# Performance work log

Hardware: AMD Instinct MI355X
Metric: run time of the kernel (lower is better)

Reference implementation:

```python
import jax, jax.numpy as jnp
import numpy as np

H = 16          # num attention heads (== num kv heads here)
D = 128         # head_dim
HID = 2048      # hidden_size = H * D
THETA = 10000.0
SCALE = 1.0 / (D ** 0.5)
EPS = 1e-8


def rotate_half(x):
    x1, x2 = x[..., : D // 2], x[..., D // 2 :]
    return jnp.concatenate((-x2, x1), axis=-1)


def rope_tables(seq_len):
    inv_freq = 1.0 / (THETA ** (jnp.arange(0, D, 2, dtype=jnp.float32) / D))
    freqs = jnp.outer(jnp.arange(seq_len, dtype=jnp.float32), inv_freq)  # [S, D/2]
    emb = jnp.concatenate((freqs, freqs), axis=-1)                        # [S, D]
    return jnp.cos(emb), jnp.sin(emb)


def setup_inputs() -> dict:
    key = jax.random.key(0)
    ks = jax.random.split(key, 10)
    B, S = 1, 2048
    hidden_states = jax.random.normal(ks[0], (B, S, HID), jnp.float32) * 0.02
    position_ids = jnp.tile(jnp.arange(S, dtype=jnp.int32)[None, :], (B, 1))
    # additive causal mask, shape (B, 1, S, S) as asserted in the torch forward
    causal = jnp.tril(jnp.ones((S, S), dtype=bool))
    attention_mask = jnp.where(causal, 0.0, -1e9).astype(jnp.float32)[None, None]
    attention_mask = jnp.tile(attention_mask, (B, 1, 1, 1))
    Wq = jax.random.normal(ks[1], (HID, HID), jnp.float32) * 0.02
    bq = jax.random.normal(ks[2], (HID,), jnp.float32) * 0.02
    Wk = jax.random.normal(ks[3], (HID, HID), jnp.float32) * 0.02
    bk = jax.random.normal(ks[4], (HID,), jnp.float32) * 0.02
    Wo = jax.random.normal(ks[5], (HID, HID), jnp.float32) * 0.02
    beta = jax.random.normal(ks[6], (1,), jnp.float32)
    M = jax.random.normal(ks[7], (H, D, D), jnp.float32) * 0.02
    z = jax.random.uniform(ks[8], (H, D), jnp.float32) * 100.0 + 1.0  # positive accumulator
    return {
        "hidden_states": hidden_states,
        "attention_mask": attention_mask,
        "position_ids": position_ids,
        "Wq": Wq, "bq": bq, "Wk": Wk, "bk": bk, "Wo": Wo,
        "beta": beta, "M": M, "z": z,
    }


def reference(hidden_states, attention_mask, position_ids, Wq, bq, Wk, bk, Wo, beta, M, z):
    B, S, _ = hidden_states.shape
    # projections (NOTE: source uses q_proj for value_states too -- reproduced faithfully)
    q = (hidden_states @ Wq + bq).reshape(B, S, H, D).transpose(0, 2, 1, 3)  # [B,H,S,D]
    k = (hidden_states @ Wk + bk).reshape(B, S, H, D).transpose(0, 2, 1, 3)
    v = q  # value_states = q_proj(hidden_states), no RoPE applied to values

    cos, sin = rope_tables(S)
    cos = cos[position_ids][:, None]  # [B,1,S,D]
    sin = sin[position_ids][:, None]
    qr = q * cos + rotate_half(q) * sin
    kr = k * cos + rotate_half(k) * sin

    # --- compressive memory retrieval (with pre-update M, z) ---
    sq = jax.nn.elu(qr) + 1.0                                  # [B,H,S,D]
    mem_num = jnp.einsum('bhsd,hde->bhse', sq, M)              # [B,H,S,D]
    mem_den = jnp.einsum('bhsd,hd->bhs', sq, z)[..., None] + EPS
    memory_output = mem_num / mem_den

    # --- memory update: outer-product accumulation ---
    sk = jax.nn.elu(kr) + 1.0
    M_new = M + jnp.einsum('bhsd,bhse->hde', sk, v)
    z_new = z + sk.sum(axis=(0, 2))

    # --- local attention (SDPA with additive mask, dropout 0) ---
    scores = jnp.einsum('bhsd,bhtd->bhst', qr, kr) * SCALE + attention_mask
    probs = jax.nn.softmax(scores, axis=-1)
    attn_output = jnp.einsum('bhst,bhtd->bhsd', probs, v)

    # --- long-term memory injection: sigmoid-gated blend ---
    g = jax.nn.sigmoid(beta)[0]
    combined = g * memory_output + (1.0 - g) * attn_output     # [B,H,S,D]
    combined = combined.transpose(0, 2, 1, 3).reshape(B, S, HID)
    final_output = combined @ Wo
    return (final_output, M_new, z_new)
```

## Files before the change

### kernel.cpp

```cpp
#include <hip/hip_runtime.h>
#include <hip/hip_bf16.h>


#define S_LEN 2048
#define HID 2048
#define NH 16
#define HD 128
#define SCALE_QK 0.088388347648318447f

typedef __attribute__((ext_vector_type(8))) short bf16x8;
typedef __attribute__((ext_vector_type(4))) float f32x4;

__device__ __forceinline__ short f2bf(float f) {
  __hip_bfloat16 h = __float2bfloat16(f);
  return __builtin_bit_cast(short, h);
}
__device__ __forceinline__ float bf2f(short s) {
  unsigned int u = ((unsigned int)(unsigned short)s) << 16;
  return __builtin_bit_cast(float, u);
}
__device__ __forceinline__ void gload16(const void* g, void* l) {
  __builtin_amdgcn_global_load_lds(
      (const __attribute__((address_space(1))) void*)g,
      (__attribute__((address_space(3))) void*)l, 16, 0, 0);
}

__global__ __launch_bounds__(256) void f32_to_bf16_kernel(
    const float* __restrict__ in, short* __restrict__ out) {
  size_t i = (size_t)(blockIdx.x * 256 + threadIdx.x) * 8;
  float4 a = *reinterpret_cast<const float4*>(in + i);
  float4 b = *reinterpret_cast<const float4*>(in + i + 4);
  alignas(16) short t[8] = {f2bf(a.x), f2bf(a.y), f2bf(a.z), f2bf(a.w),
                            f2bf(b.x), f2bf(b.y), f2bf(b.z), f2bf(b.w)};
  *reinterpret_cast<int4*>(out + i) = *reinterpret_cast<int4*>(t);
}

__global__ __launch_bounds__(256) void transpose_f2b_kernel(
    const float* __restrict__ in, short* __restrict__ out, int R, int C) {
  __shared__ float t[32][33];
  size_t bo = (size_t)blockIdx.z * R * C;
  int r0 = blockIdx.y * 32, c0 = blockIdx.x * 32;
  int tx = threadIdx.x & 31, ty = threadIdx.x >> 5;
#pragma unroll
  for (int i = 0; i < 4; ++i)
    t[ty + i * 8][tx] = in[bo + (size_t)(r0 + ty + i * 8) * C + c0 + tx];
  __syncthreads();
#pragma unroll
  for (int i = 0; i < 4; ++i)
    out[bo + (size_t)(c0 + ty + i * 8) * R + r0 + tx] = f2bf(t[tx][ty + i * 8]);
}

__global__ __launch_bounds__(256) void transpose_b2b_kernel(
    const short* __restrict__ in, short* __restrict__ out, int R, int C) {
  __shared__ short t[32][33];
  int r0 = blockIdx.y * 32, c0 = blockIdx.x * 32;
  int tx = threadIdx.x & 31, ty = threadIdx.x >> 5;
#pragma unroll
  for (int i = 0; i < 4; ++i)
    t[ty + i * 8][tx] = in[(size_t)(r0 + ty + i * 8) * C + c0 + tx];
  __syncthreads();
#pragma unroll
  for (int i = 0; i < 4; ++i)
    out[(size_t)(c0 + ty + i * 8) * R + r0 + tx] = t[tx][ty + i * 8];
}

__global__ __launch_bounds__(256) void tables_kernel(
    const int* __restrict__ pos_ids, float* __restrict__ cost,
    float* __restrict__ sint) {
  int idx = blockIdx.x * 256 + threadIdx.x;
  int s = idx >> 6, j = idx & 63;
  float pos = (float)pos_ids[s];
  float inv = powf(10000.0f, -((float)j) / 64.0f);
  float a = pos * inv;
  cost[idx] = cosf(a);
  sint[idx] = sinf(a);
}

__global__ __launch_bounds__(256) void gemm_bt_dual_kernel(
    const short* __restrict__ A, const short* __restrict__ BT,
    const float* __restrict__ bias0, const float* __restrict__ bias1,
    float* __restrict__ C0, float* __restrict__ C1) {
  __shared__ short As[128 * 64];
  __shared__ short Bs[128 * 64];
  const int K = 2048;
  const int tid = threadIdx.x;
  const int wave = tid >> 6, lane = tid & 63;
  const int g = lane >> 4, l15 = lane & 15;
  const int wm = (wave >> 1) * 64, wn = (wave & 1) * 64;
  const int row0 = blockIdx.x * 128;
  const int colg0 = blockIdx.y * 128;

  const int ld_r = wave * 32 + (lane >> 3);
  const int ld_c = (lane & 7) * 8;
  const short* Ag = A + (size_t)(row0 + ld_r) * K + ld_c;
  const short* Bg = BT + (size_t)(colg0 + ld_r) * K + ld_c;
  short* Al = As + wave * 2048;
  short* Bl = Bs + wave * 2048;

  f32x4 acc[4][4] = {};
  for (int kt = 0; kt < K; kt += 64) {
    __syncthreads();
#pragma unroll
    for (int i = 0; i < 4; ++i) {
      gload16(Ag + kt + (size_t)i * 8 * K, Al + i * 512);
      gload16(Bg + kt + (size_t)i * 8 * K, Bl + i * 512);
    }
    __syncthreads();
#pragma unroll
    for (int ks = 0; ks < 2; ++ks) {
      bf16x8 a[4], b[4];
#pragma unroll
      for (int m = 0; m < 4; ++m)
        a[m] = *reinterpret_cast<bf16x8*>(
            reinterpret_cast<char*>(As) + (wm + m * 16 + l15) * 128 +
            (ks * 32 + g * 8) * 2);
#pragma unroll
      for (int n = 0; n < 4; ++n)
        b[n] = *reinterpret_cast<bf16x8*>(
            reinterpret_cast<char*>(Bs) + (wn + n * 16 + l15) * 128 +
            (ks * 32 + g * 8) * 2);
#pragma unroll
      for (int m = 0; m < 4; ++m)
#pragma unroll
        for (int n = 0; n < 4; ++n)
          acc[m][n] = __builtin_amdgcn_mfma_f32_16x16x32_bf16(a[m], b[n],
                                                              acc[m][n], 0, 0, 0);
    }
  }

  float* C = (colg0 < 2048) ? C0 : C1;
  const float* bias = (colg0 < 2048) ? bias0 : bias1;
  const int col0 = (colg0 < 2048) ? colg0 : colg0 - 2048;
#pragma unroll
  for (int m = 0; m < 4; ++m)
#pragma unroll
    for (int n = 0; n < 4; ++n) {
      int row = row0 + wm + m * 16 + g * 4;
      int col = col0 + wn + n * 16 + l15;
      float bv = bias ? bias[col] : 0.0f;
#pragma unroll
      for (int r = 0; r < 4; ++r)
        C[(size_t)(row + r) * 2048 + col] = acc[m][n][r] + bv;
    }
}

__global__ __launch_bounds__(256) void rope_kernel(
    const float* __restrict__ qf, const float* __restrict__ kf,
    const float* __restrict__ cost, const float* __restrict__ sint,
    short* __restrict__ qr, short* __restrict__ kr, short* __restrict__ sq,
    short* __restrict__ sk, short* __restrict__ v) {
  int s = blockIdx.x;
  int hd = threadIdx.x * 8;
  int d = hd & 127;
  bool lo = d < 64;
  size_t base = (size_t)s * HID + hd;
  size_t pb = lo ? base + 64 : base - 64;
  int tb = s * 64 + (hd & 63);
  alignas(16) short oqr[8], okr[8], osq[8], osk[8], ov[8];
#pragma unroll
  for (int j = 0; j < 8; ++j) {
    float c = cost[tb + j], sn = sint[tb + j];
    float q = qf[base + j], qp = qf[pb + j];
    float k = kf[base + j], kp = kf[pb + j];
    float rq = lo ? -qp : qp;
    float rk = lo ? -kp : kp;
    float qrv = q * c + rq * sn;
    float krv = k * c + rk * sn;
    oqr[j] = f2bf(qrv);
    okr[j] = f2bf(krv);
    osq[j] = f2bf(qrv > 0.0f ? qrv + 1.0f : __expf(qrv));
    osk[j] = f2bf(krv > 0.0f ? krv + 1.0f : __expf(krv));
    ov[j] = f2bf(q);
  }
  *reinterpret_cast<int4*>(qr + base) = *reinterpret_cast<int4*>(oqr);
  *reinterpret_cast<int4*>(kr + base) = *reinterpret_cast<int4*>(okr);
  *reinterpret_cast<int4*>(sq + base) = *reinterpret_cast<int4*>(osq);
  *reinterpret_cast<int4*>(sk + base) = *reinterpret_cast<int4*>(osk);
  *reinterpret_cast<int4*>(v + base) = *reinterpret_cast<int4*>(ov);
}

__global__ __launch_bounds__(256) void attn_kernel(
    const short* __restrict__ qr, const short* __restrict__ kr,
    const short* __restrict__ vT, const short* __restrict__ sq,
    const short* __restrict__ MT, const float* __restrict__ z,
    const float* __restrict__ beta, short* __restrict__ comb) {
  __shared__ short k_s[2][64 * 128];
  __shared__ short v_s[2][128 * 64];
  __shared__ short p_s[4][16 * 64];
  const int tid = threadIdx.x;
  const int wave = tid >> 6, lane = tid & 63;
  const int g = lane >> 4, l15 = lane & 15;
  const int bid = blockIdx.x;
  const int h = bid & 15;
  const int u = bid >> 4;
  const int qt = (u < 16) ? (2 * u) : (31 - 2 * (u - 16));
  const int q0 = qt * 64;
  const int ntiles = qt + 1;

  const int krow_b = wave * 16 + (lane >> 4);
  const int vrow_b = wave * 32 + (lane >> 3);
#define STAGE_TILE(B, T0)                                                     \
  {                                                                           \
    _Pragma("unroll") for (int i = 0; i < 4; ++i) {                           \
      int rk = krow_b + i * 4;                                                \
      int ck = (lane & 15) ^ (rk & 7);                                        \
      gload16(kr + (size_t)((T0) + rk) * HID + h * HD + ck * 8,               \
              &k_s[B][0] + wave * 2048 + i * 512);                            \
      int rv = vrow_b + i * 8;                                                \
      int cv = (lane & 7) ^ (rv & 7);                                         \
      gload16(vT + (size_t)(h * HD + rv) * S_LEN + (T0) + cv * 8,             \
              &v_s[B][0] + wave * 2048 + i * 512);                            \
    }                                                                         \
  }

  bf16x8 qf[4];
#pragma unroll
  for (int ks = 0; ks < 4; ++ks) {
    int row = q0 + wave * 16 + l15;
    qf[ks] = *reinterpret_cast<const bf16x8*>(qr + (size_t)row * HID + h * HD +
                                              ks * 32 + g * 8);
  }

  STAGE_TILE(0, 0);
  __syncthreads();

  f32x4 o[8] = {};
  float m_run[4], l_run[4];
#pragma unroll
  for (int r = 0; r < 4; ++r) {
    m_run[r] = -3.0e38f;
    l_run[r] = 0.0f;
  }

  for (int kt = 0; kt < ntiles; ++kt) {
    const int cur = kt & 1;
    if (kt + 1 < ntiles) STAGE_TILE(cur ^ 1, (kt + 1) * 64);

    f32x4 sfr[4] = {};
    __builtin_amdgcn_s_setprio(1);
#pragma unroll
    for (int n = 0; n < 4; ++n) {
#pragma unroll
      for (int ks = 0; ks < 4; ++ks) {
        int rr = n * 16 + l15;
        int off = (rr * 256 + (ks * 32 + g * 8) * 2) ^ ((rr & 7) << 4);
        bf16x8 b =
            *reinterpret_cast<bf16x8*>(reinterpret_cast<char*>(k_s[cur]) + off);
        sfr[n] = __builtin_amdgcn_mfma_f32_16x16x32_bf16(qf[ks], b, sfr[n], 0,
                                                         0, 0);
      }
    }
    __builtin_amdgcn_s_setprio(0);

    const bool diag = (kt == qt);
#pragma unroll
    for (int r = 0; r < 4; ++r) {
      const int srow = q0 + wave * 16 + g * 4 + r;
      float mx = m_run[r];
#pragma unroll
      for (int n = 0; n < 4; ++n) {
        float val = sfr[n][r] * SCALE_QK;
        if (diag) {
          int t = kt * 64 + n * 16 + l15;
          val = (t <= srow) ? val : -3.0e38f;
        }
        sfr[n][r] = val;
        mx = fmaxf(mx, val);
      }
      mx = fmaxf(mx, __shfl_xor(mx, 1));
      mx = fmaxf(mx, __shfl_xor(mx, 2));
      mx = fmaxf(mx, __shfl_xor(mx, 4));
      mx = fmaxf(mx, __shfl_xor(mx, 8));
      float sum = 0.0f;
#pragma unroll
      for (int n = 0; n < 4; ++n) {
        float p = __expf(sfr[n][r] - mx);
        sfr[n][r] = p;
        sum += p;
      }
      sum += __shfl_xor(sum, 1);
      sum += __shfl_xor(sum, 2);
      sum += __shfl_xor(sum, 4);
      sum += __shfl_xor(sum, 8);
      float f = __expf(m_run[r] - mx);
      l_run[r] = l_run[r] * f + sum;
      m_run[r] = mx;
#pragma unroll
      for (int n = 0; n < 8; ++n) o[n][r] *= f;
    }

    char* pw = reinterpret_cast<char*>(p_s[wave]);
#pragma unroll
    for (int n = 0; n < 4; ++n)
#pragma unroll
      for (int r = 0; r < 4; ++r) {
        int rl = g * 4 + r;
        int off = (rl * 128 + (n * 16 + l15) * 2) ^ ((rl & 7) << 4);
        *reinterpret_cast<short*>(pw + off) = f2bf(sfr[n][r]);
      }

    __builtin_amdgcn_s_setprio(1);
#pragma unroll
    for (int ks = 0; ks < 2; ++ks) {
      int offp = (l15 * 128 + (ks * 32 + g * 8) * 2) ^ ((l15 & 7) << 4);
      bf16x8 pa = *reinterpret_cast<bf16x8*>(pw + offp);
#pragma unroll
      for (int n = 0; n < 8; ++n) {
        int rr = n * 16 + l15;
        int off = (rr * 128 + (ks * 32 + g * 8) * 2) ^ ((rr & 7) << 4);
        bf16x8 vb =
            *reinterpret_cast<bf16x8*>(reinterpret_cast<char*>(v_s[cur]) + off);
        o[n] = __builtin_amdgcn_mfma_f32_16x16x32_bf16(pa, vb, o[n], 0, 0, 0);
      }
    }
    __builtin_amdgcn_s_setprio(0);

    __syncthreads();
  }
#undef STAGE_TILE

  short* mt_s = &k_s[0][0];
#pragma unroll
  for (int i = 0; i < 8; ++i) {
    int c = tid + 256 * i;
    int r = c >> 4, kc = c & 15;
    int4 d = *reinterpret_cast<const int4*>(MT + (size_t)h * 16384 + r * 128 +
                                            kc * 8);
    *reinterpret_cast<int4*>(reinterpret_cast<char*>(mt_s) +
                             ((r * 256 + kc * 16) ^ ((r & 7) << 4))) = d;
  }
  __syncthreads();

  bf16x8 af[4];
#pragma unroll
  for (int ks = 0; ks < 4; ++ks) {
    int row = q0 + wave * 16 + l15;
    af[ks] = *reinterpret_cast<const bf16x8*>(sq + (size_t)row * HID + h * HD +
                                              ks * 32 + g * 8);
  }
  f32x4 acc2[8] = {};
#pragma unroll
  for (int ks = 0; ks < 4; ++ks) {
#pragma unroll
    for (int n = 0; n < 8; ++n) {
      int rr = n * 16 + l15;
      int off = (rr * 256 + (ks * 32 + g * 8) * 2) ^ ((rr & 7) << 4);
      bf16x8 b =
          *reinterpret_cast<bf16x8*>(reinterpret_cast<char*>(mt_s) + off);
      acc2[n] = __builtin_amdgcn_mfma_f32_16x16x32_bf16(af[ks], b, acc2[n], 0,
                                                        0, 0);
    }
  }

  float den[4];
#pragma unroll
  for (int r = 0; r < 4; ++r) {
    int row = q0 + wave * 16 + g * 4 + r;
    bf16x8 sv =
        *reinterpret_cast<const bf16x8*>(sq + (size_t)row * HID + h * HD +
                                         l15 * 8);
    float part = 0.0f;
#pragma unroll
    for (int j = 0; j < 8; ++j) part += bf2f(sv[j]) * z[h * HD + l15 * 8 + j];
    part += __shfl_xor(part, 1);
    part += __shfl_xor(part, 2);
    part += __shfl_xor(part, 4);
    part += __shfl_xor(part, 8);
    den[r] = part + 1e-8f;
  }

  float gv = 1.0f / (1.0f + __expf(-beta[0]));
#pragma unroll
  for (int n = 0; n < 8; ++n)
#pragma unroll
    for (int r = 0; r < 4; ++r) {
      int row = q0 + wave * 16 + g * 4 + r;
      int col = n * 16 + l15;
      float mem = acc2[n][r] / den[r];
      float at = o[n][r] / l_run[r];
      comb[(size_t)row * HID + h * HD + col] = f2bf(gv * mem + (1.0f - gv) * at);
    }
}

__global__ __launch_bounds__(256) void mnew_part_kernel(
    const short* __restrict__ skT, const short* __restrict__ vT,
    float* __restrict__ part) {
  const int sp = blockIdx.x;
  const int h = blockIdx.y;
  const int tid = threadIdx.x;
  const int wave = tid >> 6, lane = tid & 63;
  const int g = lane >> 4, l15 = lane & 15;
  f32x4 acc[2][8] = {};
  for (int ks = sp * 8; ks < sp * 8 + 8; ++ks) {
    bf16x8 a[2];
#pragma unroll
    for (int m = 0; m < 2; ++m) {
      int dd = wave * 32 + m * 16 + l15;
      a[m] = *reinterpret_cast<const bf16x8*>(skT + (size_t)(h * HD + dd) * S_LEN +
                                              ks * 32 + g * 8);
    }
#pragma unroll
    for (int n = 0; n < 8; ++n) {
      int e = n * 16 + l15;
      bf16x8 b = *reinterpret_cast<const bf16x8*>(
          vT + (size_t)(h * HD + e) * S_LEN + ks * 32 + g * 8);
#pragma unroll
      for (int m = 0; m < 2; ++m)
        acc[m][n] =
            __builtin_amdgcn_mfma_f32_16x16x32_bf16(a[m], b, acc[m][n], 0, 0, 0);
    }
  }
#pragma unroll
  for (int m = 0; m < 2; ++m)
#pragma unroll
    for (int n = 0; n < 8; ++n)
#pragma unroll
      for (int r = 0; r < 4; ++r) {
        int dd = wave * 32 + m * 16 + g * 4 + r;
        int e = n * 16 + l15;
        part[(size_t)(sp * 16 + h) * 16384 + (size_t)dd * 128 + e] =
            acc[m][n][r];
      }
}

__global__ __launch_bounds__(256) void mnew_reduce_kernel(
    const float* __restrict__ part, const float* __restrict__ Mold,
    float* __restrict__ Mout) {
  int idx = blockIdx.x * 256 + threadIdx.x;
  int j4 = idx * 4;
  int h = j4 >> 14;
  int rem = j4 & 16383;
  float4 a = *reinterpret_cast<const float4*>(Mold + j4);
#pragma unroll
  for (int s = 0; s < 8; ++s) {
    float4 p = *reinterpret_cast<const float4*>(
        part + ((size_t)(s * 16 + h) << 14) + rem);
    a.x += p.x;
    a.y += p.y;
    a.z += p.z;
    a.w += p.w;
  }
  *reinterpret_cast<float4*>(Mout + j4) = a;
}

__global__ __launch_bounds__(256) void znew_kernel(const short* __restrict__ skT,
                                                   const float* __restrict__ z,
                                                   float* __restrict__ out) {
  int row = blockIdx.x;
  int tid = threadIdx.x;
  bf16x8 vv = *reinterpret_cast<const bf16x8*>(skT + (size_t)row * S_LEN + tid * 8);
  float s = 0.0f;
#pragma unroll
  for (int j = 0; j < 8; ++j) s += bf2f(vv[j]);
#pragma unroll
  for (int off = 1; off < 64; off <<= 1) s += __shfl_xor(s, off);
  __shared__ float wsum[4];
  if ((tid & 63) == 0) wsum[tid >> 6] = s;
  __syncthreads();
  if (tid == 0) out[row] = z[row] + wsum[0] + wsum[1] + wsum[2] + wsum[3];
}

extern "C" void kernel_launch(void* const* d_in, const int* in_sizes, int n_in,
                              void* d_out, int out_size, void* d_ws,
                              size_t ws_size, hipStream_t stream) {
  const float* hs = (const float*)d_in[0];
  const int* pos = (const int*)d_in[2];
  const float* Wq = (const float*)d_in[3];
  const float* bq = (const float*)d_in[4];
  const float* Wk = (const float*)d_in[5];
  const float* bk = (const float*)d_in[6];
  const float* Wo = (const float*)d_in[7];
  const float* beta = (const float*)d_in[8];
  const float* Mm = (const float*)d_in[9];
  const float* z = (const float*)d_in[10];
  float* out = (float*)d_out;

  char* ws = (char*)d_ws;
  const size_t MB = 1u << 20;
  float* q_f32 = (float*)(ws + 0);
  float* k_f32 = (float*)(ws + 16 * MB);
  short* hs_b = (short*)(ws + 32 * MB);
  short* WqkT = (short*)(ws + 40 * MB);
  short* WoT = (short*)(ws + 56 * MB);
  short* qr = (short*)(ws + 64 * MB);
  short* kr = (short*)(ws + 72 * MB);
  short* sq = (short*)(ws + 80 * MB);
  short* vT = (short*)(ws + 88 * MB);
  short* MT = (short*)(ws + 96 * MB);
  float* cost = (float*)(ws + 96 * MB + 512 * 1024);
  float* sint = (float*)(ws + 97 * MB);
  short* comb = (short*)k_f32;
  short* sk = hs_b;
  short* v = WqkT;
  short* skT = WqkT + 4 * 1024 * 1024;
  float* mpart = q_f32;

  f32_to_bf16_kernel<<<2048, 256, 0, stream>>>(hs, hs_b);
  transpose_f2b_kernel<<<dim3(64, 64, 1), 256, 0, stream>>>(Wq, WqkT, 2048, 2048);
  transpose_f2b_kernel<<<dim3(64, 64, 1), 256, 0, stream>>>(
      Wk, WqkT + 4 * 1024 * 1024, 2048, 2048);
  transpose_f2b_kernel<<<dim3(64, 64, 1), 256, 0, stream>>>(Wo, WoT, 2048, 2048);
  transpose_f2b_kernel<<<dim3(4, 4, 16), 256, 0, stream>>>(Mm, MT, 128, 128);
  tables_kernel<<<512, 256, 0, stream>>>(pos, cost, sint);

  gemm_bt_dual_kernel<<<dim3(16, 32), 256, 0, stream>>>(hs_b, WqkT, bq, bk,
                                                        q_f32, k_f32);
  rope_kernel<<<2048, 256, 0, stream>>>(q_f32, k_f32, cost, sint, qr, kr, sq, sk,
                                        v);
  transpose_b2b_kernel<<<dim3(64, 64, 1), 256, 0, stream>>>(v, vT, 2048, 2048);
  transpose_b2b_kernel<<<dim3(64, 64, 1), 256, 0, stream>>>(sk, skT, 2048, 2048);

  attn_kernel<<<512, 256, 0, stream>>>(qr, kr, vT, sq, MT, z, beta, comb);
  gemm_bt_dual_kernel<<<dim3(16, 16), 256, 0, stream>>>(comb, WoT, nullptr,
                                                        nullptr, out, out);
  mnew_part_kernel<<<dim3(8, 16), 256, 0, stream>>>(skT, vT, mpart);
  mnew_reduce_kernel<<<256, 256, 0, stream>>>(mpart, Mm, out + 4194304);
  znew_kernel<<<2048, 256, 0, stream>>>(skT, z, out + 4194304 + 16 * 128 * 128);
}
```

Measured before the change: 362.1 us.

## Fuse RoPE epilogue into QK projection GEMM and double-buffer GEMM LDS loads

Folds the bias add, rotary embedding, ELU+1 feature map and bf16 conversion into the epilogue of the Q/K projection GEMM. The tile is staged through shared memory so each thread can reach its rotate-half partner, which removes the fp32 q/k round trip through global memory and one kernel launch. Both GEMMs now double-buffer their LDS tiles, prefetching the next K-slice while the current one feeds the MFMAs. The cost is 64KB+ of LDS per block, which may lower occupancy, plus a reorganised workspace layout.

```diff
diff --git a/kernel.cpp b/kernel.cpp
--- a/kernel.cpp
+++ b/kernel.cpp
@@ -76,12 +76,13 @@
   sint[idx] = sinf(a);
 }
 
-__global__ __launch_bounds__(256) void gemm_bt_dual_kernel(
+__global__ __launch_bounds__(256) void gemm_qk_rope_kernel(
     const short* __restrict__ A, const short* __restrict__ BT,
-    const float* __restrict__ bias0, const float* __restrict__ bias1,
-    float* __restrict__ C0, float* __restrict__ C1) {
-  __shared__ short As[128 * 64];
-  __shared__ short Bs[128 * 64];
+    const float* __restrict__ bq, const float* __restrict__ bk,
+    const float* __restrict__ cost, const float* __restrict__ sint,
+    short* __restrict__ qr, short* __restrict__ kr, short* __restrict__ sq,
+    short* __restrict__ sk, short* __restrict__ v) {
+  __shared__ __align__(16) char smem[67584];
   const int K = 2048;
   const int tid = threadIdx.x;
   const int wave = tid >> 6, lane = tid & 63;
@@ -94,31 +95,36 @@
   const int ld_c = (lane & 7) * 8;
   const short* Ag = A + (size_t)(row0 + ld_r) * K + ld_c;
   const short* Bg = BT + (size_t)(colg0 + ld_r) * K + ld_c;
-  short* Al = As + wave * 2048;
-  short* Bl = Bs + wave * 2048;
+
+#define GSTAGE(BUF, KT)                                                       \
+  {                                                                           \
+    _Pragma("unroll") for (int i = 0; i < 4; ++i) {                           \
+      gload16(Ag + (size_t)(KT) * 64 + (size_t)i * 8 * 2048,                  \
+              smem + (BUF) * 32768 + wave * 4096 + i * 1024);                 \
+      gload16(Bg + (size_t)(KT) * 64 + (size_t)i * 8 * 2048,                  \
+              smem + (BUF) * 32768 + 16384 + wave * 4096 + i * 1024);         \
+    }                                                                         \
+  }
 
   f32x4 acc[4][4] = {};
-  for (int kt = 0; kt < K; kt += 64) {
-    __syncthreads();
-#pragma unroll
-    for (int i = 0; i < 4; ++i) {
-      gload16(Ag + kt + (size_t)i * 8 * K, Al + i * 512);
-      gload16(Bg + kt + (size_t)i * 8 * K, Bl + i * 512);
-    }
-    __syncthreads();
+  GSTAGE(0, 0);
+  __syncthreads();
+  for (int kt = 0; kt < 32; ++kt) {
+    const int cur = kt & 1;
+    if (kt + 1 < 32) GSTAGE(cur ^ 1, kt + 1);
 #pragma unroll
     for (int ks = 0; ks < 2; ++ks) {
       bf16x8 a[4], b[4];
 #pragma unroll
       for (int m = 0; m < 4; ++m)
-        a[m] = *reinterpret_cast<bf16x8*>(
-            reinterpret_cast<char*>(As) + (wm + m * 16 + l15) * 128 +
-            (ks * 32 + g * 8) * 2);
+        a[m] = *reinterpret_cast<bf16x8*>(smem + cur * 32768 +
+                                          (wm + m * 16 + l15) * 128 +
+                                          (ks * 32 + g * 8) * 2);
 #pragma unroll
       for (int n = 0; n < 4; ++n)
-        b[n] = *reinterpret_cast<bf16x8*>(
-            reinterpret_cast<char*>(Bs) + (wn + n * 16 + l15) * 128 +
-            (ks * 32 + g * 8) * 2);
+        b[n] = *reinterpret_cast<bf16x8*>(smem + cur * 32768 + 16384 +
+                                          (wn + n * 16 + l15) * 128 +
+                                          (ks * 32 + g * 8) * 2);
 #pragma unroll
       for (int m = 0; m < 4; ++m)
 #pragma unroll
@@ -126,57 +132,124 @@
           acc[m][n] = __builtin_amdgcn_mfma_f32_16x16x32_bf16(a[m], b[n],
                                                               acc[m][n], 0, 0, 0);
     }
-  }
-
-  float* C = (colg0 < 2048) ? C0 : C1;
-  const float* bias = (colg0 < 2048) ? bias0 : bias1;
-  const int col0 = (colg0 < 2048) ? colg0 : colg0 - 2048;
+    __syncthreads();
+  }
+#undef GSTAGE
+
+  const bool qpath = (colg0 < 2048);
+  const int col0 = qpath ? colg0 : colg0 - 2048;
+  const float* bias = qpath ? bq : bk;
+  float* qb = reinterpret_cast<float*>(smem);
+#pragma unroll
+  for (int m = 0; m < 4; ++m)
+#pragma unroll
+    for (int n = 0; n < 4; ++n) {
+      int rl = wm + m * 16 + g * 4;
+      int cl = wn + n * 16 + l15;
+      float bv = bias[col0 + cl];
+#pragma unroll
+      for (int r = 0; r < 4; ++r) qb[(rl + r) * 132 + cl] = acc[m][n][r] + bv;
+    }
+  __syncthreads();
+
+  const int rl = tid >> 1;
+  const int c0 = (tid & 1) * 64;
+  const int rowg = row0 + rl;
+  const float sgn = (c0 == 0) ? -1.0f : 1.0f;
+  const size_t obase = (size_t)rowg * HID + col0 + c0;
+#pragma unroll
+  for (int j0 = 0; j0 < 64; j0 += 8) {
+    alignas(16) short o1[8], o2[8], o3[8];
+#pragma unroll
+    for (int jj = 0; jj < 8; ++jj) {
+      int j = j0 + jj;
+      float self = qb[rl * 132 + c0 + j];
+      float part = qb[rl * 132 + (c0 ^ 64) + j];
+      float cs = cost[rowg * 64 + j];
+      float sn = sint[rowg * 64 + j];
+      float rv = self * cs + sgn * part * sn;
+      o1[jj] = f2bf(rv);
+      o2[jj] = f2bf(rv > 0.0f ? rv + 1.0f : __expf(rv));
+      o3[jj] = f2bf(self);
+    }
+    if (qpath) {
+      *reinterpret_cast<int4*>(qr + obase + j0) = *reinterpret_cast<int4*>(o1);
+      *reinterpret_cast<int4*>(sq + obase + j0) = *reinterpret_cast<int4*>(o2);
+      *reinterpret_cast<int4*>(v + obase + j0) = *reinterpret_cast<int4*>(o3);
+    } else {
+      *reinterpret_cast<int4*>(kr + obase + j0) = *reinterpret_cast<int4*>(o1);
+      *reinterpret_cast<int4*>(sk + obase + j0) = *reinterpret_cast<int4*>(o2);
+    }
+  }
+}
+
+__global__ __launch_bounds__(256) void gemm_wo_kernel(
+    const short* __restrict__ A, const short* __restrict__ BT,
+    float* __restrict__ C) {
+  __shared__ __align__(16) char smem[65536];
+  const int K = 2048;
+  const int tid = threadIdx.x;
+  const int wave = tid >> 6, lane = tid & 63;
+  const int g = lane >> 4, l15 = lane & 15;
+  const int wm = (wave >> 1) * 64, wn = (wave & 1) * 64;
+  const int row0 = blockIdx.x * 128;
+  const int col0 = blockIdx.y * 128;
+
+  const int ld_r = wave * 32 + (lane >> 3);
+  const int ld_c = (lane & 7) * 8;
+  const short* Ag = A + (size_t)(row0 + ld_r) * K + ld_c;
+  const short* Bg = BT + (size_t)(col0 + ld_r) * K + ld_c;
+
+#define GSTAGE(BUF, KT)                                                       \
+  {                                                                           \
+    _Pragma("unroll") for (int i = 0; i < 4; ++i) {                           \
+      gload16(Ag + (size_t)(KT) * 64 + (size_t)i * 8 * 2048,                  \
+              smem + (BUF) * 32768 + wave * 4096 + i * 1024);                 \
+      gload16(Bg + (size_t)(KT) * 64 + (size_t)i * 8 * 2048,                  \
+              smem + (BUF) * 32768 + 16384 + wave * 4096 + i * 1024);         \
+    }                                                                         \
+  }
+
+  f32x4 acc[4][4] = {};
+  GSTAGE(0, 0);
+  __syncthreads();
+  for (int kt = 0; kt < 32; ++kt) {
+    const int cur = kt & 1;
+    if (kt + 1 < 32) GSTAGE(cur ^ 1, kt + 1);
+#pragma unroll
+    for (int ks = 0; ks < 2; ++ks) {
+      bf16x8 a[4], b[4];
+#pragma unroll
+      for (int m = 0; m < 4; ++m)
+        a[m] = *reinterpret_cast<bf16x8*>(smem + cur * 32768 +
+                                          (wm + m * 16 + l15) * 128 +
+                                          (ks * 32 + g * 8) * 2);
+#pragma unroll
+      for (int n = 0; n < 4; ++n)
+        b[n] = *reinterpret_cast<bf16x8*>(smem + cur * 32768 + 16384 +
+                                          (wn + n * 16 + l15) * 128 +
+                                          (ks * 32 + g * 8) * 2);
+#pragma unroll
+      for (int m = 0; m < 4; ++m)
+#pragma unroll
+        for (int n = 0; n < 4; ++n)
+          acc[m][n] = __builtin_amdgcn_mfma_f32_16x16x32_bf16(a[m], b[n],
+                                                              acc[m][n], 0, 0, 0);
+    }
+    __syncthreads();
+  }
+#undef GSTAGE
+
 #pragma unroll
   for (int m = 0; m < 4; ++m)
 #pragma unroll
     for (int n = 0; n < 4; ++n) {
       int row = row0 + wm + m * 16 + g * 4;
       int col = col0 + wn + n * 16 + l15;
-      float bv = bias ? bias[col] : 0.0f;
 #pragma unroll
       for (int r = 0; r < 4; ++r)
-        C[(size_t)(row + r) * 2048 + col] = acc[m][n][r] + bv;
-    }
-}
-
-__global__ __launch_bounds__(256) void rope_kernel(
-    const float* __restrict__ qf, const float* __restrict__ kf,
-    const float* __restrict__ cost, const float* __restrict__ sint,
-    short* __restrict__ qr, short* __restrict__ kr, short* __restrict__ sq,
-    short* __restrict__ sk, short* __restrict__ v) {
-  int s = blockIdx.x;
-  int hd = threadIdx.x * 8;
-  int d = hd & 127;
-  bool lo = d < 64;
-  size_t base = (size_t)s * HID + hd;
-  size_t pb = lo ? base + 64 : base - 64;
-  int tb = s * 64 + (hd & 63);
-  alignas(16) short oqr[8], okr[8], osq[8], osk[8], ov[8];
-#pragma unroll
-  for (int j = 0; j < 8; ++j) {
-    float c = cost[tb + j], sn = sint[tb + j];
-    float q = qf[base + j], qp = qf[pb + j];
-    float k = kf[base + j], kp = kf[pb + j];
-    float rq = lo ? -qp : qp;
-    float rk = lo ? -kp : kp;
-    float qrv = q * c + rq * sn;
-    float krv = k * c + rk * sn;
-    oqr[j] = f2bf(qrv);
-    okr[j] = f2bf(krv);
-    osq[j] = f2bf(qrv > 0.0f ? qrv + 1.0f : __expf(qrv));
-    osk[j] = f2bf(krv > 0.0f ? krv + 1.0f : __expf(krv));
-    ov[j] = f2bf(q);
-  }
-  *reinterpret_cast<int4*>(qr + base) = *reinterpret_cast<int4*>(oqr);
-  *reinterpret_cast<int4*>(kr + base) = *reinterpret_cast<int4*>(okr);
-  *reinterpret_cast<int4*>(sq + base) = *reinterpret_cast<int4*>(osq);
-  *reinterpret_cast<int4*>(sk + base) = *reinterpret_cast<int4*>(osk);
-  *reinterpret_cast<int4*>(v + base) = *reinterpret_cast<int4*>(ov);
+        C[(size_t)(row + r) * 2048 + col] = acc[m][n][r];
+    }
 }
 
 __global__ __launch_bounds__(256) void attn_kernel(
@@ -356,9 +429,8 @@
 #pragma unroll
   for (int r = 0; r < 4; ++r) {
     int row = q0 + wave * 16 + g * 4 + r;
-    bf16x8 sv =
-        *reinterpret_cast<const bf16x8*>(sq + (size_t)row * HID + h * HD +
-                                         l15 * 8);
+    bf16x8 sv = *reinterpret_cast<const bf16x8*>(sq + (size_t)row * HID +
+                                                 h * HD + l15 * 8);
     float part = 0.0f;
 #pragma unroll
     for (int j = 0; j < 8; ++j) part += bf2f(sv[j]) * z[h * HD + l15 * 8 + j];
@@ -477,23 +549,21 @@
 
   char* ws = (char*)d_ws;
   const size_t MB = 1u << 20;
-  float* q_f32 = (float*)(ws + 0);
-  float* k_f32 = (float*)(ws + 16 * MB);
-  short* hs_b = (short*)(ws + 32 * MB);
-  short* WqkT = (short*)(ws + 40 * MB);
-  short* WoT = (short*)(ws + 56 * MB);
-  short* qr = (short*)(ws + 64 * MB);
-  short* kr = (short*)(ws + 72 * MB);
-  short* sq = (short*)(ws + 80 * MB);
-  short* vT = (short*)(ws + 88 * MB);
-  short* MT = (short*)(ws + 96 * MB);
-  float* cost = (float*)(ws + 96 * MB + 512 * 1024);
-  float* sint = (float*)(ws + 97 * MB);
-  short* comb = (short*)k_f32;
-  short* sk = hs_b;
-  short* v = WqkT;
-  short* skT = WqkT + 4 * 1024 * 1024;
-  float* mpart = q_f32;
+  short* hs_b = (short*)(ws + 0);
+  short* WqkT = (short*)(ws + 8 * MB);
+  short* WoT = (short*)(ws + 24 * MB);
+  short* qr = (short*)(ws + 32 * MB);
+  short* kr = (short*)(ws + 40 * MB);
+  short* sq = (short*)(ws + 48 * MB);
+  short* sk = (short*)(ws + 56 * MB);
+  short* v = (short*)(ws + 64 * MB);
+  short* comb = (short*)(ws + 72 * MB);
+  short* MT = (short*)(ws + 80 * MB);
+  float* cost = (float*)(ws + 80 * MB + 512 * 1024);
+  float* sint = (float*)(ws + 81 * MB);
+  short* skT = WqkT;
+  short* vT = WqkT + 4 * 1024 * 1024;
+  float* mpart = (float*)hs_b;
 
   f32_to_bf16_kernel<<<2048, 256, 0, stream>>>(hs, hs_b);
   transpose_f2b_kernel<<<dim3(64, 64, 1), 256, 0, stream>>>(Wq, WqkT, 2048, 2048);
@@ -503,16 +573,13 @@
   transpose_f2b_kernel<<<dim3(4, 4, 16), 256, 0, stream>>>(Mm, MT, 128, 128);
   tables_kernel<<<512, 256, 0, stream>>>(pos, cost, sint);
 
-  gemm_bt_dual_kernel<<<dim3(16, 32), 256, 0, stream>>>(hs_b, WqkT, bq, bk,
-                                                        q_f32, k_f32);
-  rope_kernel<<<2048, 256, 0, stream>>>(q_f32, k_f32, cost, sint, qr, kr, sq, sk,
-                                        v);
+  gemm_qk_rope_kernel<<<dim3(16, 32), 256, 0, stream>>>(
+      hs_b, WqkT, bq, bk, cost, sint, qr, kr, sq, sk, v);
   transpose_b2b_kernel<<<dim3(64, 64, 1), 256, 0, stream>>>(v, vT, 2048, 2048);
   transpose_b2b_kernel<<<dim3(64, 64, 1), 256, 0, stream>>>(sk, skT, 2048, 2048);
 
   attn_kernel<<<512, 256, 0, stream>>>(qr, kr, vT, sq, MT, z, beta, comb);
-  gemm_bt_dual_kernel<<<dim3(16, 16), 256, 0, stream>>>(comb, WoT, nullptr,
-                                                        nullptr, out, out);
+  gemm_wo_kernel<<<dim3(16, 16), 256, 0, stream>>>(comb, WoT, out);
   mnew_part_kernel<<<dim3(8, 16), 256, 0, stream>>>(skT, vT, mpart);
   mnew_reduce_kernel<<<256, 256, 0, stream>>>(mpart, Mm, out + 4194304);
   znew_kernel<<<2048, 256, 0, stream>>>(skT, z, out + 4194304 + 16 * 128 * 128);
```

Result: no change. 356.8 us (-1.5%).
